# Performance work log

Measured on AMD Instinct MI355X. Metric: run time of the kernel, lower is better.

The kernel has to match this reference:

```python
import jax, jax.numpy as jnp
import numpy as np

N, K, C, S = 32768, 16, 64, 8
EPS = 1e-5

def _bn(x, g, b):
    # BatchNorm1d in training mode: normalize over all axes except channel (last)
    axes = tuple(range(x.ndim - 1))
    m = x.mean(axes, keepdims=True)
    v = x.var(axes, keepdims=True)
    return (x - m) * jax.lax.rsqrt(v + EPS) * g + b

def setup_inputs() -> dict:
    key = jax.random.key(0)
    ks = jax.random.split(key, 24)
    def W(k, i, o):
        return (jax.random.normal(k, (i, o), jnp.float32) * 0.02)
    d = {}
    d['xyz'] = jax.random.normal(ks[0], (N, 3), jnp.float32)
    d['features'] = jax.random.normal(ks[1], (N, C), jnp.float32)
    d['velocities'] = jax.random.normal(ks[2], (N, 1), jnp.float32)
    # q/k/v projections
    d['wq'] = W(ks[3], C, C); d['bq'] = jnp.zeros((C,), jnp.float32)
    d['wk'] = W(ks[4], C, C); d['bk'] = jnp.zeros((C,), jnp.float32)
    d['wv'] = W(ks[5], C, C); d['bv'] = jnp.zeros((C,), jnp.float32)
    # linear_p: Linear(3,3) -> BN(3) -> ReLU -> Linear(3,C)
    d['p1_w'] = W(ks[6], 3, 3); d['p1_b'] = jnp.zeros((3,), jnp.float32)
    d['p_bn_g'] = jnp.ones((3,), jnp.float32); d['p_bn_b'] = jnp.zeros((3,), jnp.float32)
    d['p2_w'] = W(ks[7], 3, C); d['p2_b'] = jnp.zeros((C,), jnp.float32)
    # velocity encoder: Linear(1,1) -> BN(1) -> ReLU -> Linear(1,C)
    d['v1_w'] = W(ks[8], 1, 1); d['v1_b'] = jnp.zeros((1,), jnp.float32)
    d['v_bn_g'] = jnp.ones((1,), jnp.float32); d['v_bn_b'] = jnp.zeros((1,), jnp.float32)
    d['v2_w'] = W(ks[9], 1, C); d['v2_b'] = jnp.zeros((C,), jnp.float32)
    # linear_w: BN(C) -> ReLU -> Linear(C, C//S) -> BN(C//S) -> ReLU -> Linear(C//S, C//S)
    d['w_bn1_g'] = jnp.ones((C,), jnp.float32); d['w_bn1_b'] = jnp.zeros((C,), jnp.float32)
    d['w1_w'] = W(ks[10], C, C // S); d['w1_b'] = jnp.zeros((C // S,), jnp.float32)
    d['w_bn2_g'] = jnp.ones((C // S,), jnp.float32); d['w_bn2_b'] = jnp.zeros((C // S,), jnp.float32)
    d['w2_w'] = W(ks[11], C // S, C // S); d['w2_b'] = jnp.zeros((C // S,), jnp.float32)
    # rho: BN(C) -> ReLU -> Linear(C, C)
    d['rho_bn_g'] = jnp.ones((C,), jnp.float32); d['rho_bn_b'] = jnp.zeros((C,), jnp.float32)
    d['rho_w'] = W(ks[12], C, C); d['rho_b'] = jnp.zeros((C,), jnp.float32)
    # precomputed KNN neighbor indices (coordinate-space and velocity-space)
    d['idx'] = jax.random.randint(ks[13], (N, K), 0, N, jnp.int32)
    d['idx_v'] = jax.random.randint(ks[14], (N, K), 0, N, jnp.int32)
    return d

def reference(xyz, features, velocities, wq, bq, wk, bk, wv, bv,
              p1_w, p1_b, p_bn_g, p_bn_b, p2_w, p2_b,
              v1_w, v1_b, v_bn_g, v_bn_b, v2_w, v2_b,
              w_bn1_g, w_bn1_b, w1_w, w1_b, w_bn2_g, w_bn2_b, w2_w, w2_b,
              rho_bn_g, rho_bn_b, rho_w, rho_b, idx, idx_v):
    x_q = features @ wq + bq                      # [N,C]
    x_k = features @ wk + bk
    x_v = features @ wv + bv
    # queryandgroup: gather neighbors; relative coords prepended for k-path
    p_r = xyz[idx] - xyz[:, None, :]              # [N,K,3]
    x_k_g = x_k[idx]                              # [N,K,C]
    x_v_g = x_v[idx]                              # [N,K,C]
    # positional encoder
    p_enc = jax.nn.relu(_bn(p_r @ p1_w + p1_b, p_bn_g, p_bn_b)) @ p2_w + p2_b   # [N,K,C]
    # velocity encoder (KNN in velocity space)
    v_g = velocities[idx_v]                        # [N,K,1]
    v_enc = jax.nn.relu(_bn(v_g @ v1_w + v1_b, v_bn_g, v_bn_b)) @ v2_w + v2_b   # [N,K,C]
    # subtraction attention scoring
    w = x_k_g - x_q[:, None, :] + (p_enc + v_enc)  # [N,K,C]
    w = jax.nn.relu(_bn(w, w_bn1_g, w_bn1_b)) @ w1_w + w1_b
    w = jax.nn.relu(_bn(w, w_bn2_g, w_bn2_b)) @ w2_w + w2_b   # [N,K,C//S]
    w = jax.nn.softmax(w, axis=1)                  # softmax over neighbors
    # grouped weighted sum with share_planes
    a = (x_v_g + p_enc + v_enc).reshape(N, K, S, C // S)
    out = (a * w[:, :, None, :]).sum(axis=1).reshape(N, C)
    out = out + features
    out = jax.nn.relu(_bn(out, rho_bn_g, rho_bn_b)) @ rho_w + rho_b
    return out
```

## Files before the change

### kernel.cpp

```cpp
#include <hip/hip_runtime.h>

#define NPTS 32768
#define KNN 16
#define CH 64
#define CS 8
#define NKP (NPTS*KNN)
#define EPSBN 1e-5f

#define G1 1024
#define G2 2048
#define G3 2048
#define G4 2048
#define G5 1024

template<int CTRL>
__device__ __forceinline__ float dppf(float x){
  int r = __builtin_amdgcn_update_dpp(0, __float_as_int(x), CTRL, 0xf, 0xf, true);
  return __int_as_float(r);
}
__device__ __forceinline__ float dpp_sum16(float x){
  x += dppf<0xB1>(x); x += dppf<0x4E>(x); x += dppf<0x141>(x); x += dppf<0x140>(x);
  return x;
}
__device__ __forceinline__ float dpp_max16(float x){
  x = fmaxf(x, dppf<0xB1>(x)); x = fmaxf(x, dppf<0x4E>(x));
  x = fmaxf(x, dppf<0x141>(x)); x = fmaxf(x, dppf<0x140>(x));
  return x;
}

struct EncParams {
  float q00,q01,q02,q10,q11,q12,q20,q21,q22;
  float pb0,pb1,pb2;
  float ps0,ps1,ps2, pt0,pt1,pt2;
  float v1w, v1b, vs, vt;
};

__device__ __forceinline__ EncParams load_enc(const float* __restrict__ p1w, const float* __restrict__ p1b,
                                              const float* __restrict__ v1w, const float* __restrict__ v1b,
                                              const float* __restrict__ stats) {
  EncParams P;
  P.q00=p1w[0]; P.q01=p1w[1]; P.q02=p1w[2];
  P.q10=p1w[3]; P.q11=p1w[4]; P.q12=p1w[5];
  P.q20=p1w[6]; P.q21=p1w[7]; P.q22=p1w[8];
  P.pb0=p1b[0]; P.pb1=p1b[1]; P.pb2=p1b[2];
  P.ps0=stats[0]; P.ps1=stats[1]; P.ps2=stats[2];
  P.pt0=stats[3]; P.pt1=stats[4]; P.pt2=stats[5];
  P.v1w=v1w[0]; P.v1b=v1b[0]; P.vs=stats[6]; P.vt=stats[7];
  return P;
}

__device__ __forceinline__ void enc_scalars(const EncParams& P, const float* __restrict__ xyz,
                                            const float* __restrict__ vel, int m, int mv,
                                            float xn0, float xn1, float xn2,
                                            float& ry0, float& ry1, float& ry2, float& rv) {
  float pr0 = xyz[m*3+0]-xn0, pr1 = xyz[m*3+1]-xn1, pr2 = xyz[m*3+2]-xn2;
  float y0 = pr0*P.q00 + pr1*P.q10 + pr2*P.q20 + P.pb0;
  float y1 = pr0*P.q01 + pr1*P.q11 + pr2*P.q21 + P.pb1;
  float y2 = pr0*P.q02 + pr1*P.q12 + pr2*P.q22 + P.pb2;
  ry0 = fmaxf(y0*P.ps0+P.pt0, 0.f);
  ry1 = fmaxf(y1*P.ps1+P.pt1, 0.f);
  ry2 = fmaxf(y2*P.ps2+P.pt2, 0.f);
  float vr = vel[mv]*P.v1w + P.v1b;
  rv = fmaxf(vr*P.vs+P.vt, 0.f);
}

__global__ __launch_bounds__(256) void k1_qkv_stats(
    const float* __restrict__ feat,
    const float* __restrict__ wq, const float* __restrict__ bq,
    const float* __restrict__ wk, const float* __restrict__ bk,
    const float* __restrict__ wv, const float* __restrict__ bv,
    const float* __restrict__ xyz, const float* __restrict__ vel,
    const float* __restrict__ p1w, const float* __restrict__ p1b,
    const float* __restrict__ v1w, const float* __restrict__ v1b,
    const int* __restrict__ idx, const int* __restrict__ idxv,
    float* __restrict__ xq, float* __restrict__ xk, float* __restrict__ xv,
    float* __restrict__ part1)
{
  __shared__ __attribute__((aligned(16))) float4 lw4[3072];
  __shared__ __attribute__((aligned(16))) float lf[2048];
  __shared__ float red1[32];
  float* lw = (float*)lw4;
  int tid = threadIdx.x;
  for (int i = tid; i < 3072; i += 256) {
    float4 v;
    if (i < 1024) v = ((const float4*)wq)[i];
    else if (i < 2048) v = ((const float4*)wk)[i-1024];
    else v = ((const float4*)wv)[i-2048];
    lw4[i] = v;
  }
  __syncthreads();
  int lane = tid & 63, wave = tid >> 6;
  int nb = blockIdx.x*32 + wave*8;
  #pragma unroll
  for (int r=0;r<8;r++)
    lf[wave*512 + r*64 + lane] = feat[(nb+r)*64 + lane];
  float aq[8], ak[8], av[8];
  #pragma unroll
  for (int r=0;r<8;r++){ aq[r]=0.f; ak[r]=0.f; av[r]=0.f; }
  for (int i=0;i<64;i+=4){
    float4 fr[8];
    #pragma unroll
    for (int r=0;r<8;r++) fr[r] = *(const float4*)&lf[wave*512 + r*64 + i];
    #pragma unroll
    for (int ii=0;ii<4;ii++){
      float wqi = lw[(i+ii)*64+lane];
      float wki = lw[4096+(i+ii)*64+lane];
      float wvi = lw[8192+(i+ii)*64+lane];
      #pragma unroll
      for (int r=0;r<8;r++){
        float f = ii==0?fr[r].x: ii==1?fr[r].y: ii==2?fr[r].z: fr[r].w;
        aq[r] += f*wqi; ak[r] += f*wki; av[r] += f*wvi;
      }
    }
  }
  float bql=bq[lane], bkl=bk[lane], bvl=bv[lane];
  #pragma unroll
  for (int r=0;r<8;r++){
    int row = nb + r;
    xq[row*64+lane] = aq[r]+bql;
    xk[row*64+lane] = ak[r]+bkl;
    xv[row*64+lane] = av[r]+bvl;
  }
  float q00=p1w[0],q01=p1w[1],q02=p1w[2],q10=p1w[3],q11=p1w[4],q12=p1w[5],q20=p1w[6],q21=p1w[7],q22=p1w[8];
  float pb0=p1b[0],pb1=p1b[1],pb2=p1b[2];
  float v1w_=v1w[0], v1b_=v1b[0];
  float s0=0,s1=0,s2=0,sv=0,t0=0,t1=0,t2=0,tv=0;
  int gid = blockIdx.x*256 + tid;
  #pragma unroll
  for (int rep=0; rep<2; rep++){
    int p = gid + rep*(G1*256);
    int n = p >> 4;
    int m = idx[p], mv = idxv[p];
    float xn0=xyz[n*3], xn1=xyz[n*3+1], xn2=xyz[n*3+2];
    float pr0=xyz[m*3]-xn0, pr1=xyz[m*3+1]-xn1, pr2=xyz[m*3+2]-xn2;
    float y0 = pr0*q00+pr1*q10+pr2*q20+pb0;
    float y1 = pr0*q01+pr1*q11+pr2*q21+pb1;
    float y2 = pr0*q02+pr1*q12+pr2*q22+pb2;
    float vr = vel[mv]*v1w_ + v1b_;
    s0+=y0; s1+=y1; s2+=y2; sv+=vr;
    t0+=y0*y0; t1+=y1*y1; t2+=y2*y2; tv+=vr*vr;
  }
  #pragma unroll
  for (int msk=1; msk<64; msk<<=1){
    s0 += __shfl_xor(s0,msk); s1 += __shfl_xor(s1,msk); s2 += __shfl_xor(s2,msk); sv += __shfl_xor(sv,msk);
    t0 += __shfl_xor(t0,msk); t1 += __shfl_xor(t1,msk); t2 += __shfl_xor(t2,msk); tv += __shfl_xor(tv,msk);
  }
  if (lane==0){
    red1[wave*8+0]=s0; red1[wave*8+1]=s1; red1[wave*8+2]=s2; red1[wave*8+3]=sv;
    red1[wave*8+4]=t0; red1[wave*8+5]=t1; red1[wave*8+6]=t2; red1[wave*8+7]=tv;
  }
  __syncthreads();
  if (tid < 8){
    float a = red1[tid] + red1[8+tid] + red1[16+tid] + red1[24+tid];
    part1[blockIdx.x*8 + tid] = a;
  }
}

__global__ __launch_bounds__(1024) void r1_finalize(
    const float* __restrict__ P, const float* __restrict__ pg, const float* __restrict__ pb,
    const float* __restrict__ vg, const float* __restrict__ vb, float* __restrict__ stats)
{
  constexpr int COLG = 2, NSL = 1024/COLG, ITER = G1/NSL;
  __shared__ float4 red[1024];
  int t = threadIdx.x; int cg = t % COLG, sl = t / COLG;
  float4 acc = make_float4(0.f,0.f,0.f,0.f);
  const float4* P4 = (const float4*)P;
  #pragma unroll
  for (int j=0;j<ITER;j++){
    int i = sl + j*NSL;
    float4 v = P4[i*COLG + cg];
    acc.x+=v.x; acc.y+=v.y; acc.z+=v.z; acc.w+=v.w;
  }
  red[t] = acc; __syncthreads();
  for (int off = NSL/2; off>0; off>>=1){
    if (sl < off){
      float4 o = red[(sl+off)*COLG + cg];
      acc.x+=o.x; acc.y+=o.y; acc.z+=o.z; acc.w+=o.w;
      red[sl*COLG + cg] = acc;
    }
    __syncthreads();
  }
  if (t<4){
    float s = ((float*)red)[t];
    float q = ((float*)red)[4+t];
    float inv = 1.f/(float)NKP;
    float mean=s*inv, var=q*inv-mean*mean;
    float g = (t<3)? pg[t]:vg[0];
    float b = (t<3)? pb[t]:vb[0];
    float sc = g*rsqrtf(var+EPSBN);
    float sh = b - mean*sc;
    if (t<3){ stats[t]=sc; stats[3+t]=sh; } else { stats[6]=sc; stats[7]=sh; }
  }
}

__global__ __launch_bounds__(256) void k1b_renc(
    const float* __restrict__ xyz, const float* __restrict__ vel,
    const float* __restrict__ p1w, const float* __restrict__ p1b,
    const float* __restrict__ v1w, const float* __restrict__ v1b,
    const int* __restrict__ idx, const int* __restrict__ idxv,
    const float* __restrict__ stats, float* __restrict__ renc)
{
  EncParams P = load_enc(p1w,p1b,v1w,v1b,stats);
  int p = blockIdx.x*256 + threadIdx.x;
  int n = p >> 4;
  int m = idx[p], mv = idxv[p];
  float ry0,ry1,ry2,rv;
  enc_scalars(P, xyz, vel, m, mv, xyz[n*3], xyz[n*3+1], xyz[n*3+2], ry0,ry1,ry2,rv);
  ((float4*)renc)[p] = make_float4(ry0,ry1,ry2,rv);
}

template<int NB, int NCH>
__global__ __launch_bounds__(1024) void finalize_bn_t(
    const float* __restrict__ P, float inv,
    const float* __restrict__ g, const float* __restrict__ b,
    float* __restrict__ oscale, float* __restrict__ oshift)
{
  constexpr int COLS = 2*NCH;
  constexpr int COLG = COLS/4;
  constexpr int NSL  = 1024/COLG;
  constexpr int ITER = NB/NSL;
  __shared__ float4 red[1024];
  int t = threadIdx.x; int cg = t % COLG, sl = t / COLG;
  float4 acc = make_float4(0.f,0.f,0.f,0.f);
  const float4* P4 = (const float4*)P;
  #pragma unroll 8
  for (int j=0;j<ITER;j++){
    int i = sl + j*NSL;
    float4 v = P4[i*COLG + cg];
    acc.x+=v.x; acc.y+=v.y; acc.z+=v.z; acc.w+=v.w;
  }
  red[t] = acc; __syncthreads();
  for (int off = NSL/2; off>0; off>>=1){
    if (sl < off){
      float4 o = red[(sl+off)*COLG + cg];
      acc.x+=o.x; acc.y+=o.y; acc.z+=o.z; acc.w+=o.w;
      red[sl*COLG + cg] = acc;
    }
    __syncthreads();
  }
  if (t < NCH){
    float s = ((float*)red)[t];
    float q = ((float*)red)[NCH + t];
    float mean=s*inv, var=q*inv-mean*mean;
    float sc=g[t]*rsqrtf(var+EPSBN);
    oscale[t]=sc; oshift[t]=b[t]-mean*sc;
  }
}

__global__ __launch_bounds__(256) void k2_wstats(
    const int* __restrict__ idx, const float* __restrict__ renc,
    const float* __restrict__ p2w, const float* __restrict__ p2b,
    const float* __restrict__ v2w, const float* __restrict__ v2b,
    const float* __restrict__ xq, const float* __restrict__ xk,
    float* __restrict__ part2)
{
  int tid = threadIdx.x;
  int lane = tid & 63, wave = tid >> 6;
  float A = p2w[lane], B = p2w[64+lane], C2 = p2w[128+lane];
  float D = v2w[lane], E = p2b[lane] + v2b[lane];
  const float4* renc4 = (const float4*)renc;
  float sum=0.f, ssq=0.f;
  int gw = blockIdx.x*4 + wave;
  for (int n0 = gw; n0 < NPTS; n0 += G2*4){
    int nu = __builtin_amdgcn_readfirstlane(n0);
    float xqc = xq[nu*64+lane];
    #pragma unroll 4
    for (int k=0;k<KNN;k++){
      int pu = nu*KNN + k;
      int m = idx[pu];
      float4 rr = renc4[pu];
      float e = rr.x*A + rr.y*B + rr.z*C2 + rr.w*D + E;
      float w = xk[m*64+lane] - xqc + e;
      sum += w; ssq += w*w;
    }
  }
  __shared__ float rs[4][64], rq[4][64];
  rs[wave][lane]=sum; rq[wave][lane]=ssq;
  __syncthreads();
  if (tid < 64){
    float s = rs[0][tid]+rs[1][tid]+rs[2][tid]+rs[3][tid];
    float q = rq[0][tid]+rq[1][tid]+rq[2][tid]+rq[3][tid];
    part2[blockIdx.x*128 + tid] = s;
    part2[blockIdx.x*128 + 64 + tid] = q;
  }
}

__global__ __launch_bounds__(256) void k3_w1(
    const float* __restrict__ p2w, const float* __restrict__ p2b,
    const float* __restrict__ v2w, const float* __restrict__ v2b,
    const float* __restrict__ w1w, const float* __restrict__ w1b,
    const int* __restrict__ idx, const float* __restrict__ renc,
    const float* __restrict__ xq, const float* __restrict__ xk,
    const float* __restrict__ stats,
    float* __restrict__ w1o, float* __restrict__ part3)
{
  __shared__ __attribute__((aligned(16))) float coef[64*20];
  __shared__ float rs[256], rq[256];
  int tid=threadIdx.x;
  if (tid < 64){
    int c = tid;
    int slot = ((c&7)<<3) | (c>>3);
    float* cf = &coef[slot*20];
    cf[0]=p2w[c]; cf[1]=p2w[64+c]; cf[2]=p2w[128+c];
    cf[3]=v2w[c]; cf[4]=p2b[c]+v2b[c];
    cf[5]=stats[8+c]; cf[6]=stats[72+c];
    #pragma unroll
    for (int j=0;j<8;j++) cf[7+j]=w1w[c*8+j];
    #pragma unroll
    for (int j=15;j<20;j++) cf[j]=0.f;
  }
  __syncthreads();
  int lane=tid&63, wave=tid>>6;
  int sl = lane&7, sp = lane>>3;
  bool p4 = (sl&4)==0, p1 = (sl&1)==0, p2 = (sl&2)==0;
  int jmap = (sl&4) | ((sl&1)<<1) | ((sl&2)>>1);
  float w1b_l = w1b[jmap];
  const float4* renc4=(const float4*)renc;
  const float4* xk4=(const float4*)xk;
  const float4* xq4=(const float4*)xq;
  float ssum=0.f, sqq=0.f;
  int gw = blockIdx.x*4 + wave;
  for (int it = gw; it < NKP/32; it += G3*4){
    int pbase = it*32 + sp*4;
    int n = pbase >> 4;
    int4 mi = *(const int4*)&idx[pbase];
    float4 rrs[4] = {renc4[pbase+0], renc4[pbase+1], renc4[pbase+2], renc4[pbase+3]};
    float4 xqa = xq4[n*16 + sl*2], xqb = xq4[n*16 + sl*2 + 1];
    float xqv[8] = {xqa.x,xqa.y,xqa.z,xqa.w, xqb.x,xqb.y,xqb.z,xqb.w};
    float xkv[4][8];
    {
      int mm[4] = {mi.x, mi.y, mi.z, mi.w};
      #pragma unroll
      for (int u=0;u<4;u++){
        float4 a = xk4[mm[u]*16 + sl*2], b = xk4[mm[u]*16 + sl*2 + 1];
        xkv[u][0]=a.x; xkv[u][1]=a.y; xkv[u][2]=a.z; xkv[u][3]=a.w;
        xkv[u][4]=b.x; xkv[u][5]=b.y; xkv[u][6]=b.z; xkv[u][7]=b.w;
      }
    }
    float h[4][8];
    #pragma unroll
    for (int u=0;u<4;u++)
      #pragma unroll
      for (int j=0;j<8;j++) h[u][j]=0.f;
    #pragma unroll
    for (int r=0;r<8;r++){
      const float* cf = &coef[(r*8+sl)*20];
      float4 ca = *(const float4*)(cf+0);
      float4 cb = *(const float4*)(cf+4);
      float4 cc = *(const float4*)(cf+8);
      float4 cd = *(const float4*)(cf+12);
      #pragma unroll
      for (int u=0;u<4;u++){
        float e = rrs[u].x*ca.x + rrs[u].y*ca.y + rrs[u].z*ca.z + rrs[u].w*ca.w + cb.x;
        float w = xkv[u][r] - xqv[r] + e;
        float rw = fmaxf(w*cb.y + cb.z, 0.f);
        h[u][0] += rw*cb.w; h[u][1] += rw*cc.x; h[u][2] += rw*cc.y; h[u][3] += rw*cc.z;
        h[u][4] += rw*cc.w; h[u][5] += rw*cd.x; h[u][6] += rw*cd.y; h[u][7] += rw*cd.z;
      }
    }
    #pragma unroll
    for (int u=0;u<4;u++){
      float g0 = (p4? h[u][0]:h[u][4]) + dppf<0x141>(p4? h[u][4]:h[u][0]);
      float g1 = (p4? h[u][1]:h[u][5]) + dppf<0x141>(p4? h[u][5]:h[u][1]);
      float g2 = (p4? h[u][2]:h[u][6]) + dppf<0x141>(p4? h[u][6]:h[u][2]);
      float g3 = (p4? h[u][3]:h[u][7]) + dppf<0x141>(p4? h[u][7]:h[u][3]);
      float f0 = (p1? g0:g2) + dppf<0xB1>(p1? g2:g0);
      float f1 = (p1? g1:g3) + dppf<0xB1>(p1? g3:g1);
      float S  = (p2? f0:f1) + dppf<0x4E>(p2? f1:f0);
      float o = S + w1b_l;
      w1o[(pbase+u)*8 + jmap] = o;
      ssum += o; sqq += o*o;
    }
  }
  rs[(tid & ~7) | jmap]=ssum; rq[(tid & ~7) | jmap]=sqq;
  __syncthreads();
  if (tid < 8){
    float s=0.f,q=0.f;
    #pragma unroll 8
    for (int i=0;i<32;i++){ s+=rs[i*8+tid]; q+=rq[i*8+tid]; }
    part3[blockIdx.x*16 + tid] = s;
    part3[blockIdx.x*16 + 8 + tid] = q;
  }
}

__global__ __launch_bounds__(256) void k4_agg(
    const float* __restrict__ feat,
    const float* __restrict__ p2w, const float* __restrict__ p2b,
    const float* __restrict__ v2w, const float* __restrict__ v2b,
    const float* __restrict__ w2w, const float* __restrict__ w2b,
    const int* __restrict__ idx, const float* __restrict__ renc,
    const float* __restrict__ xv, const float* __restrict__ w1o,
    const float* __restrict__ stats,
    float* __restrict__ outpre, float* __restrict__ part4)
{
  __shared__ float sm_s[4][16][8];
  __shared__ float rs[4][64], rq[4][64];
  int tid=threadIdx.x, lane=tid&63, wave=tid>>6;
  int kq = lane & 15, jh = lane >> 4;
  float s2[8], t2[8];
  #pragma unroll
  for (int i=0;i<8;i++){ s2[i]=stats[136+i]; t2[i]=stats[144+i]; }
  float w2c0[8], w2c1[8];
  #pragma unroll
  for (int i=0;i<8;i++){ w2c0[i]=w2w[i*8+jh]; w2c1[i]=w2w[i*8+jh+4]; }
  float w2b0=w2b[jh], w2b1=w2b[jh+4];
  float A=p2w[lane], B=p2w[64+lane], C2=p2w[128+lane], D=v2w[lane], E=p2b[lane]+v2b[lane];
  int j = lane & 7;
  const float4* renc4 = (const float4*)renc;
  float sr=0.f, sq2=0.f;
  int gw = blockIdx.x*4 + wave;
  for (int n0 = gw; n0 < NPTS; n0 += G4*4){
    int nu = __builtin_amdgcn_readfirstlane(n0);
    const float* w1p = &w1o[(nu*KNN + kq)*8];
    float4 wa = *(const float4*)w1p;
    float4 wb = *(const float4*)(w1p+4);
    float r0 = fmaxf(wa.x*s2[0]+t2[0],0.f);
    float r1 = fmaxf(wa.y*s2[1]+t2[1],0.f);
    float r2 = fmaxf(wa.z*s2[2]+t2[2],0.f);
    float r3 = fmaxf(wa.w*s2[3]+t2[3],0.f);
    float r4 = fmaxf(wb.x*s2[4]+t2[4],0.f);
    float r5 = fmaxf(wb.y*s2[5]+t2[5],0.f);
    float r6 = fmaxf(wb.z*s2[6]+t2[6],0.f);
    float r7 = fmaxf(wb.w*s2[7]+t2[7],0.f);
    float g0 = r0*w2c0[0]+r1*w2c0[1]+r2*w2c0[2]+r3*w2c0[3]
             + r4*w2c0[4]+r5*w2c0[5]+r6*w2c0[6]+r7*w2c0[7] + w2b0;
    float g1 = r0*w2c1[0]+r1*w2c1[1]+r2*w2c1[2]+r3*w2c1[3]
             + r4*w2c1[4]+r5*w2c1[5]+r6*w2c1[6]+r7*w2c1[7] + w2b1;
    float m0 = dpp_max16(g0), m1 = dpp_max16(g1);
    float e0=__expf(g0-m0), e1=__expf(g1-m1);
    float d0 = dpp_sum16(e0), d1 = dpp_sum16(e1);
    sm_s[wave][kq][jh]   = e0/d0;
    sm_s[wave][kq][jh+4] = e1/d1;
    __asm__ __volatile__("" ::: "memory");
    float acc=0.f;
    #pragma unroll 4
    for (int k=0;k<KNN;k++){
      int pu = nu*KNN+k;
      int m = idx[pu];
      float4 rr = renc4[pu];
      float e = rr.x*A + rr.y*B + rr.z*C2 + rr.w*D + E;
      acc += (xv[m*64+lane] + e) * sm_s[wave][k][j];
    }
    float o = acc + feat[nu*64+lane];
    outpre[nu*64+lane] = o;
    sr += o; sq2 += o*o;
    __asm__ __volatile__("" ::: "memory");
  }
  rs[wave][lane]=sr; rq[wave][lane]=sq2;
  __syncthreads();
  if (tid<64){
    float s=rs[0][tid]+rs[1][tid]+rs[2][tid]+rs[3][tid];
    float q=rq[0][tid]+rq[1][tid]+rq[2][tid]+rq[3][tid];
    part4[blockIdx.x*128+tid]=s;
    part4[blockIdx.x*128+64+tid]=q;
  }
}

__global__ __launch_bounds__(256) void k5_rho(
    const float* __restrict__ outpre, const float* __restrict__ stats,
    const float* __restrict__ rhow, const float* __restrict__ rhob,
    float* __restrict__ out)
{
  __shared__ __attribute__((aligned(16))) float4 lw4[1024];
  __shared__ __attribute__((aligned(16))) float lf[2048];
  float* lw = (float*)lw4;
  int tid=threadIdx.x;
  for (int i=tid;i<1024;i+=256) lw4[i] = ((const float4*)rhow)[i];
  __syncthreads();
  int lane=tid&63, wave=tid>>6;
  int nb = blockIdx.x*32 + wave*8;
  float scl = stats[152+lane], sft = stats[216+lane];
  #pragma unroll
  for (int r=0;r<8;r++){
    float a = outpre[(nb+r)*64+lane];
    lf[wave*512 + r*64 + lane] = fmaxf(a*scl+sft, 0.f);
  }
  float acc[8];
  #pragma unroll
  for (int r=0;r<8;r++) acc[r]=0.f;
  for (int i=0;i<64;i+=4){
    float4 fr[8];
    #pragma unroll
    for (int r=0;r<8;r++) fr[r] = *(const float4*)&lf[wave*512 + r*64 + i];
    #pragma unroll
    for (int ii=0;ii<4;ii++){
      float w_ = lw[(i+ii)*64+lane];
      #pragma unroll
      for (int r=0;r<8;r++){
        float f = ii==0?fr[r].x: ii==1?fr[r].y: ii==2?fr[r].z: fr[r].w;
        acc[r] += f*w_;
      }
    }
  }
  float bl = rhob[lane];
  #pragma unroll
  for (int r=0;r<8;r++) out[(nb+r)*64+lane] = acc[r] + bl;
}

extern "C" void kernel_launch(void* const* d_in, const int* in_sizes, int n_in,
                              void* d_out, int out_size, void* d_ws, size_t ws_size,
                              hipStream_t stream) {
  const float* xyz  = (const float*)d_in[0];
  const float* feat = (const float*)d_in[1];
  const float* vel  = (const float*)d_in[2];
  const float* wq   = (const float*)d_in[3];  const float* bq = (const float*)d_in[4];
  const float* wk   = (const float*)d_in[5];  const float* bk = (const float*)d_in[6];
  const float* wv   = (const float*)d_in[7];  const float* bv = (const float*)d_in[8];
  const float* p1w  = (const float*)d_in[9];  const float* p1b = (const float*)d_in[10];
  const float* pbg  = (const float*)d_in[11]; const float* pbb = (const float*)d_in[12];
  const float* p2w  = (const float*)d_in[13]; const float* p2b = (const float*)d_in[14];
  const float* v1w  = (const float*)d_in[15]; const float* v1b = (const float*)d_in[16];
  const float* vbg  = (const float*)d_in[17]; const float* vbb = (const float*)d_in[18];
  const float* v2w  = (const float*)d_in[19]; const float* v2b = (const float*)d_in[20];
  const float* wbn1g= (const float*)d_in[21]; const float* wbn1b= (const float*)d_in[22];
  const float* w1w  = (const float*)d_in[23]; const float* w1b = (const float*)d_in[24];
  const float* wbn2g= (const float*)d_in[25]; const float* wbn2b= (const float*)d_in[26];
  const float* w2w  = (const float*)d_in[27]; const float* w2b = (const float*)d_in[28];
  const float* rbg  = (const float*)d_in[29]; const float* rbb = (const float*)d_in[30];
  const float* rhow = (const float*)d_in[31]; const float* rhob = (const float*)d_in[32];
  const int* idx    = (const int*)d_in[33];
  const int* idxv   = (const int*)d_in[34];

  float* ws = (float*)d_ws;
  float* xq     = ws;
  float* xk     = xq + (size_t)NPTS*CH;
  float* xv     = xk + (size_t)NPTS*CH;
  float* w1o    = xv + (size_t)NPTS*CH;
  float* outpre = w1o + (size_t)NKP*CS;
  float* renc   = outpre + (size_t)NPTS*CH;
  float* part1  = renc + (size_t)NKP*4;
  float* part2  = part1 + G1*8;
  float* part3  = part2 + (size_t)G2*128;
  float* part4  = part3 + G3*16;
  float* stats  = part4 + (size_t)G4*128;

  k1_qkv_stats<<<dim3(G1), dim3(256), 0, stream>>>(
      feat, wq,bq,wk,bk,wv,bv, xyz, vel, p1w,p1b,v1w,v1b, idx, idxv, xq,xk,xv, part1);
  r1_finalize<<<dim3(1), dim3(1024), 0, stream>>>(part1, pbg,pbb, vbg,vbb, stats);
  k1b_renc<<<dim3(NKP/256), dim3(256), 0, stream>>>(
      xyz, vel, p1w,p1b, v1w,v1b, idx, idxv, stats, renc);
  k2_wstats<<<dim3(G2), dim3(256), 0, stream>>>(
      idx, renc, p2w,p2b,v2w,v2b, xq, xk, part2);
  finalize_bn_t<G2,64><<<dim3(1), dim3(1024), 0, stream>>>(
      part2, 1.f/(float)NKP, wbn1g, wbn1b, stats+8, stats+72);
  k3_w1<<<dim3(G3), dim3(256), 0, stream>>>(
      p2w,p2b,v2w,v2b, w1w,w1b, idx, renc, xq, xk, stats, w1o, part3);
  finalize_bn_t<G3,8><<<dim3(1), dim3(1024), 0, stream>>>(
      part3, 1.f/(float)NKP, wbn2g, wbn2b, stats+136, stats+144);
  k4_agg<<<dim3(G4), dim3(256), 0, stream>>>(
      feat, p2w,p2b,v2w,v2b, w2w,w2b, idx, renc, xv, w1o, stats, outpre, part4);
  finalize_bn_t<G4,64><<<dim3(1), dim3(1024), 0, stream>>>(
      part4, 1.f/(float)NPTS, rbg, rbb, stats+152, stats+216);
  k5_rho<<<dim3(G5), dim3(256), 0, stream>>>(outpre, stats, rhow, rhob, (float*)d_out);

  (void)in_sizes; (void)n_in; (void)out_size; (void)ws_size;
}
```

Measured before the change: 153.7 us.

## Specialize waves in QKV kernel and keep weight columns in registers

The fused QKV/statistics kernel no longer stages all three 64x64 weight matrices in shared memory. Waves 0-2 each take one projection (Q, K or V), hold that matrix's 64-element weight column in registers, and compute all 32 rows of the block from a shared feature tile. Wave 3 alone computes the positional and velocity BN partial sums, which removes the cross-wave shared-memory reduction. This cuts shared memory from about 57KB to 8KB to allow higher occupancy, in exchange for higher register pressure, an uneven split between GEMM waves and the stats wave, and a __syncthreads placed inside divergent branches.

```diff
diff --git a/kernel.cpp b/kernel.cpp
--- a/kernel.cpp
+++ b/kernel.cpp
@@ -76,83 +76,70 @@
     float* __restrict__ xq, float* __restrict__ xk, float* __restrict__ xv,
     float* __restrict__ part1)
 {
-  __shared__ __attribute__((aligned(16))) float4 lw4[3072];
   __shared__ __attribute__((aligned(16))) float lf[2048];
-  __shared__ float red1[32];
-  float* lw = (float*)lw4;
-  int tid = threadIdx.x;
-  for (int i = tid; i < 3072; i += 256) {
-    float4 v;
-    if (i < 1024) v = ((const float4*)wq)[i];
-    else if (i < 2048) v = ((const float4*)wk)[i-1024];
-    else v = ((const float4*)wv)[i-2048];
-    lw4[i] = v;
-  }
-  __syncthreads();
-  int lane = tid & 63, wave = tid >> 6;
-  int nb = blockIdx.x*32 + wave*8;
-  #pragma unroll
-  for (int r=0;r<8;r++)
-    lf[wave*512 + r*64 + lane] = feat[(nb+r)*64 + lane];
-  float aq[8], ak[8], av[8];
-  #pragma unroll
-  for (int r=0;r<8;r++){ aq[r]=0.f; ak[r]=0.f; av[r]=0.f; }
-  for (int i=0;i<64;i+=4){
-    float4 fr[8];
-    #pragma unroll
-    for (int r=0;r<8;r++) fr[r] = *(const float4*)&lf[wave*512 + r*64 + i];
-    #pragma unroll
-    for (int ii=0;ii<4;ii++){
-      float wqi = lw[(i+ii)*64+lane];
-      float wki = lw[4096+(i+ii)*64+lane];
-      float wvi = lw[8192+(i+ii)*64+lane];
-      #pragma unroll
-      for (int r=0;r<8;r++){
-        float f = ii==0?fr[r].x: ii==1?fr[r].y: ii==2?fr[r].z: fr[r].w;
-        aq[r] += f*wqi; ak[r] += f*wki; av[r] += f*wvi;
+  int tid = threadIdx.x, lane = tid & 63, wave = tid >> 6;
+  int nb = blockIdx.x*32;
+  {
+    const float4* f4 = (const float4*)(feat + (size_t)nb*64);
+    float4* l4 = (float4*)lf;
+    l4[tid] = f4[tid];
+    l4[tid+256] = f4[tid+256];
+  }
+  if (wave < 3){
+    const float* wmat = wave==0? wq : wave==1? wk : wv;
+    float wcol[64];
+    #pragma unroll
+    for (int i=0;i<64;i++) wcol[i] = wmat[i*64+lane];
+    const float* bias = wave==0? bq : wave==1? bk : bv;
+    float bl = bias[lane];
+    float* outp = wave==0? xq : wave==1? xk : xv;
+    __syncthreads();
+    #pragma unroll
+    for (int t=0;t<4;t++){
+      float acc[8];
+      #pragma unroll
+      for (int r=0;r<8;r++) acc[r]=0.f;
+      #pragma unroll
+      for (int i=0;i<64;i+=4){
+        #pragma unroll
+        for (int r=0;r<8;r++){
+          float4 f = *(const float4*)&lf[(t*8+r)*64 + i];
+          acc[r] += f.x*wcol[i] + f.y*wcol[i+1] + f.z*wcol[i+2] + f.w*wcol[i+3];
+        }
       }
-    }
-  }
-  float bql=bq[lane], bkl=bk[lane], bvl=bv[lane];
-  #pragma unroll
-  for (int r=0;r<8;r++){
-    int row = nb + r;
-    xq[row*64+lane] = aq[r]+bql;
-    xk[row*64+lane] = ak[r]+bkl;
-    xv[row*64+lane] = av[r]+bvl;
-  }
-  float q00=p1w[0],q01=p1w[1],q02=p1w[2],q10=p1w[3],q11=p1w[4],q12=p1w[5],q20=p1w[6],q21=p1w[7],q22=p1w[8];
-  float pb0=p1b[0],pb1=p1b[1],pb2=p1b[2];
-  float v1w_=v1w[0], v1b_=v1b[0];
-  float s0=0,s1=0,s2=0,sv=0,t0=0,t1=0,t2=0,tv=0;
-  int gid = blockIdx.x*256 + tid;
-  #pragma unroll
-  for (int rep=0; rep<2; rep++){
-    int p = gid + rep*(G1*256);
-    int n = p >> 4;
-    int m = idx[p], mv = idxv[p];
-    float xn0=xyz[n*3], xn1=xyz[n*3+1], xn2=xyz[n*3+2];
-    float pr0=xyz[m*3]-xn0, pr1=xyz[m*3+1]-xn1, pr2=xyz[m*3+2]-xn2;
-    float y0 = pr0*q00+pr1*q10+pr2*q20+pb0;
-    float y1 = pr0*q01+pr1*q11+pr2*q21+pb1;
-    float y2 = pr0*q02+pr1*q12+pr2*q22+pb2;
-    float vr = vel[mv]*v1w_ + v1b_;
-    s0+=y0; s1+=y1; s2+=y2; sv+=vr;
-    t0+=y0*y0; t1+=y1*y1; t2+=y2*y2; tv+=vr*vr;
-  }
-  #pragma unroll
-  for (int msk=1; msk<64; msk<<=1){
-    s0 += __shfl_xor(s0,msk); s1 += __shfl_xor(s1,msk); s2 += __shfl_xor(s2,msk); sv += __shfl_xor(sv,msk);
-    t0 += __shfl_xor(t0,msk); t1 += __shfl_xor(t1,msk); t2 += __shfl_xor(t2,msk); tv += __shfl_xor(tv,msk);
-  }
-  if (lane==0){
-    red1[wave*8+0]=s0; red1[wave*8+1]=s1; red1[wave*8+2]=s2; red1[wave*8+3]=sv;
-    red1[wave*8+4]=t0; red1[wave*8+5]=t1; red1[wave*8+6]=t2; red1[wave*8+7]=tv;
-  }
-  __syncthreads();
-  if (tid < 8){
-    float a = red1[tid] + red1[8+tid] + red1[16+tid] + red1[24+tid];
-    part1[blockIdx.x*8 + tid] = a;
+      #pragma unroll
+      for (int r=0;r<8;r++) outp[(size_t)(nb+t*8+r)*64+lane] = acc[r]+bl;
+    }
+  } else {
+    float q00=p1w[0],q01=p1w[1],q02=p1w[2],q10=p1w[3],q11=p1w[4],q12=p1w[5],q20=p1w[6],q21=p1w[7],q22=p1w[8];
+    float pb0=p1b[0],pb1=p1b[1],pb2=p1b[2];
+    float v1w_=v1w[0], v1b_=v1b[0];
+    float s0=0,s1=0,s2=0,sv=0,t0=0,t1=0,t2=0,tv=0;
+    #pragma unroll
+    for (int rep=0; rep<8; rep++){
+      int p = blockIdx.x*512 + rep*64 + lane;
+      int n = p >> 4;
+      int m = idx[p], mv = idxv[p];
+      float xn0=xyz[n*3], xn1=xyz[n*3+1], xn2=xyz[n*3+2];
+      float pr0=xyz[m*3]-xn0, pr1=xyz[m*3+1]-xn1, pr2=xyz[m*3+2]-xn2;
+      float y0 = pr0*q00+pr1*q10+pr2*q20+pb0;
+      float y1 = pr0*q01+pr1*q11+pr2*q21+pb1;
+      float y2 = pr0*q02+pr1*q12+pr2*q22+pb2;
+      float vr = vel[mv]*v1w_ + v1b_;
+      s0+=y0; s1+=y1; s2+=y2; sv+=vr;
+      t0+=y0*y0; t1+=y1*y1; t2+=y2*y2; tv+=vr*vr;
+    }
+    #pragma unroll
+    for (int msk=1; msk<64; msk<<=1){
+      s0 += __shfl_xor(s0,msk); s1 += __shfl_xor(s1,msk); s2 += __shfl_xor(s2,msk); sv += __shfl_xor(sv,msk);
+      t0 += __shfl_xor(t0,msk); t1 += __shfl_xor(t1,msk); t2 += __shfl_xor(t2,msk); tv += __shfl_xor(tv,msk);
+    }
+    if (lane==0){
+      float* pp = &part1[blockIdx.x*8];
+      pp[0]=s0; pp[1]=s1; pp[2]=s2; pp[3]=sv;
+      pp[4]=t0; pp[5]=t1; pp[6]=t2; pp[7]=tv;
+    }
+    __syncthreads();
   }
 }
 
```

New measurement: 159.5 us. 1.04x slower.
